# Kernel optimization log

Measured on AMD Instinct MI355X. Metric: run time of the kernel, lower is better.

## Reference

```python
import jax, jax.numpy as jnp
import numpy as np
import math

H = 128      # hidden_size
B = 4        # bsz
N = 32       # bsz * num_doc_per_q
L = 128      # doc_len


def setup_inputs() -> dict:
    key = jax.random.key(0)
    ks = jax.random.split(key, 7)
    word_ent_info = jax.random.normal(ks[0], (N, L, H), dtype=jnp.float32)
    word_ent_info_mask = jax.random.randint(ks[1], (N, L), 0, 2, dtype=jnp.int32)
    doc = jax.random.normal(ks[2], (N, L, H), dtype=jnp.float32)
    doc_mask = jax.random.randint(ks[3], (N, L), 0, 2, dtype=jnp.int32)
    q_for_text = jax.random.normal(ks[4], (B, H), dtype=jnp.float32)
    # nn.Linear(3H, H): weight [H, 3H], bias [H]
    W1 = jax.random.normal(ks[5], (H, 3 * H), dtype=jnp.float32) / math.sqrt(3 * H)
    b1 = jnp.zeros((H,), dtype=jnp.float32)
    # nn.Linear(H, 1): weight [1, H], bias [1]
    w2 = jax.random.normal(ks[6], (1, H), dtype=jnp.float32) / math.sqrt(H)
    b2 = jnp.zeros((1,), dtype=jnp.float32)
    return {"word_ent_info": word_ent_info, "word_ent_info_mask": word_ent_info_mask,
            "doc": doc, "doc_mask": doc_mask, "q_for_text": q_for_text,
            "W1": W1, "b1": b1, "w2": w2, "b2": b2}


def reference(word_ent_info, word_ent_info_mask, doc, doc_mask, q_for_text, W1, b1, w2, b2):
    n, l, h = doc.shape
    bsz = q_for_text.shape[0]
    dt = doc.dtype

    # word_ent_infoagg = mask^T @ word_ent_info -> [N, H]
    m = word_ent_info_mask.astype(dt)
    ent_agg = jnp.einsum('nl,nlh->nh', m, word_ent_info)

    # q expanded to one row per document: [N, H]
    q_exp = jnp.repeat(q_for_text, n // bsz, axis=0)

    # Split W1 over the concat([doc_self, ent_agg, q_agg]) feature axis.
    # score_pre[n,j,k,:] = W1a @ (doc_j*doc_k) + W1b @ (doc_j*ent_agg) + W1c @ (doc_k*q)
    W1a, W1b, W1c = jnp.split(W1, 3, axis=1)        # each [H, H]
    A = jnp.einsum('nje,nke,ge->njkg', doc, doc, W1a)          # [N,L,L,H]
    Bt = jnp.einsum('nje,ge->njg', doc * ent_agg[:, None, :], W1b)  # [N,L,H]
    Ct = jnp.einsum('nke,ge->nkg', doc * q_exp[:, None, :], W1c)    # [N,L,H]
    hid = jnp.tanh(A + Bt[:, :, None, :] + Ct[:, None, :, :] + b1)  # [N,L,L,H]

    score = (jnp.einsum('njkg,g->njk', hid, w2[0]) + b2[0]) / math.sqrt(h)

    dm = doc_mask.astype(dt)
    score_mask = dm[:, :, None] * dm[:, None, :]     # [N,L,L]
    score = jnp.where(score_mask == 0.0, jnp.asarray(-1e9, dt), score)
    w = jax.nn.softmax(score, axis=-1) * score_mask
    doc_ent_enc = jnp.einsum('njk,nkh->njh', w, doc)  # [N,L,H]
    return doc_ent_enc
```

## Files before the change

kernel.cpp:

```cpp
#include <hip/hip_runtime.h>
#include <hip/hip_bf16.h>
#include <math.h>

#define Hh 128
#define Nn 32
#define Ll 128
#define W1S 384
#define PAD 136

typedef __attribute__((ext_vector_type(8))) short short8;
typedef __attribute__((ext_vector_type(4))) float floatx4;

__device__ __forceinline__ unsigned short f2bf(float x) {
  __hip_bfloat16 h = __float2bfloat16(x);
  return __builtin_bit_cast(unsigned short, h);
}
__device__ __forceinline__ float bf2f(short s) {
  unsigned int u = ((unsigned int)(unsigned short)s) << 16;
  return __builtin_bit_cast(float, u);
}
__device__ __forceinline__ short8 pack8(float4 a, float4 b) {
  short8 r;
  r[0] = (short)f2bf(a.x); r[1] = (short)f2bf(a.y);
  r[2] = (short)f2bf(a.z); r[3] = (short)f2bf(a.w);
  r[4] = (short)f2bf(b.x); r[5] = (short)f2bf(b.y);
  r[6] = (short)f2bf(b.z); r[7] = (short)f2bf(b.w);
  return r;
}

__launch_bounds__(256, 1)
__global__ void k_prep(const float* __restrict__ wei, const int* __restrict__ wmask,
                       const float* __restrict__ doc, const float* __restrict__ q,
                       const float* __restrict__ W1,
                       float* __restrict__ Bt, float* __restrict__ Ct) {
  __shared__ __align__(16) short docb[Hh * PAD];
  __shared__ __align__(16) short Wb[Hh * PAD];
  __shared__ __align__(16) short Wc[Hh * PAD];
  __shared__ __align__(16) float entL[Hh];
  __shared__ __align__(16) float qL[Hh];
  __shared__ __align__(16) float red[2][Hh];

  int n = blockIdx.x, tid = threadIdx.x;
  const float* docn = doc + (size_t)n * Ll * Hh;
  int e8 = (tid & 15) * 8;

#pragma unroll
  for (int p = 0; p < 8; ++p) {
    int row = p * 16 + (tid >> 4);
    const float4* dp = (const float4*)(docn + (size_t)row * Hh + e8);
    *(short8*)(docb + row * PAD + e8) = pack8(dp[0], dp[1]);
    const float4* wbp = (const float4*)(W1 + (size_t)row * W1S + Hh + e8);
    *(short8*)(Wb + row * PAD + e8) = pack8(wbp[0], wbp[1]);
    const float4* wcp = (const float4*)(W1 + (size_t)row * W1S + 2 * Hh + e8);
    *(short8*)(Wc + row * PAD + e8) = pack8(wcp[0], wcp[1]);
  }
  {
    int e = tid & 127, half = tid >> 7;
    const float* wp = wei + (size_t)n * Ll * Hh + (size_t)half * 64 * Hh + e;
    const int* mp = wmask + n * Ll + half * 64;
    float a = 0.f;
#pragma unroll 8
    for (int l = 0; l < 64; ++l) a = fmaf((float)mp[l], wp[(size_t)l * Hh], a);
    red[half][e] = a;
  }
  if (tid < Hh) qL[tid] = q[(n >> 3) * Hh + tid];
  __syncthreads();
  if (tid < Hh) entL[tid] = red[0][tid] + red[1][tid];
  __syncthreads();

  int lane = tid & 63, w = tid >> 6;
  int l15 = lane & 15, quad = lane >> 4;

  float ef[32], qf[32];
#pragma unroll
  for (int c = 0; c < 4; ++c)
#pragma unroll
    for (int i = 0; i < 8; ++i) {
      int e = c * 32 + quad * 8 + i;
      ef[c * 8 + i] = entL[e];
      qf[c * 8 + i] = qL[e];
    }
  short8 draw[2][4];
#pragma unroll
  for (int mt = 0; mt < 2; ++mt)
#pragma unroll
    for (int c = 0; c < 4; ++c)
      draw[mt][c] = *(const short8*)(docb + (w * 32 + mt * 16 + l15) * PAD + c * 32 + quad * 8);

  for (int which = 0; which < 2; ++which) {
    const short* Ws = which ? Wc : Wb;
    const float* sf = which ? qf : ef;
    floatx4 acc[2][8];
#pragma unroll
    for (int mt = 0; mt < 2; ++mt)
#pragma unroll
      for (int nt = 0; nt < 8; ++nt) acc[mt][nt] = (floatx4){0.f, 0.f, 0.f, 0.f};
#pragma unroll
    for (int c = 0; c < 4; ++c) {
      short8 af[2];
#pragma unroll
      for (int mt = 0; mt < 2; ++mt) {
        float t[8];
#pragma unroll
        for (int i = 0; i < 8; ++i) t[i] = bf2f(draw[mt][c][i]) * sf[c * 8 + i];
        short8 r;
#pragma unroll
        for (int i = 0; i < 8; ++i) r[i] = (short)f2bf(t[i]);
        af[mt] = r;
      }
      short8 bfr[8];
#pragma unroll
      for (int nt = 0; nt < 8; ++nt)
        bfr[nt] = *(const short8*)(Ws + (nt * 16 + l15) * PAD + c * 32 + quad * 8);
#pragma unroll
      for (int mt = 0; mt < 2; ++mt)
#pragma unroll
        for (int nt = 0; nt < 8; ++nt)
          acc[mt][nt] = __builtin_amdgcn_mfma_f32_16x16x32_bf16(af[mt], bfr[nt], acc[mt][nt], 0, 0, 0);
    }
    float* outp = (which ? Ct : Bt) + (size_t)n * Ll * Hh;
#pragma unroll
    for (int mt = 0; mt < 2; ++mt)
#pragma unroll
      for (int nt = 0; nt < 8; ++nt)
#pragma unroll
        for (int r = 0; r < 4; ++r) {
          int k = w * 32 + mt * 16 + quad * 4 + r;
          outp[(size_t)k * Hh + nt * 16 + l15] = acc[mt][nt][r];
        }
  }
}

__launch_bounds__(256, 2)
__global__ void k_main(const float* __restrict__ doc, const int* __restrict__ dmask,
                       const float* __restrict__ W1, const float* __restrict__ b1,
                       const float* __restrict__ w2, const float* __restrict__ b2,
                       const float* __restrict__ Bt, const float* __restrict__ Ct,
                       float* __restrict__ out) {
  __shared__ __align__(16) short As[Hh * PAD];
  __shared__ __align__(16) short Bs[Hh * PAD];
  __shared__ __align__(16) float sc[Ll];
  __shared__ __align__(16) float scw[Ll];

  int bid = blockIdx.x;
  int n = bid & 31, j = bid >> 5;
  int tid = threadIdx.x;
  const float* docn = doc + (size_t)n * Ll * Hh;
  size_t orow = ((size_t)n * Ll + j) * Hh;

  if (dmask[n * Ll + j] == 0) {
    if (tid < Hh) out[orow + tid] = 0.f;
    return;
  }

  int e8 = (tid & 15) * 8;
  const float4* jp = (const float4*)(docn + (size_t)j * Hh + e8);
  float4 j0 = jp[0], j1 = jp[1];
#pragma unroll
  for (int p = 0; p < 8; ++p) {
    int row = p * 16 + (tid >> 4);
    const float4* wp = (const float4*)(W1 + (size_t)row * W1S + e8);
    *(short8*)(As + row * PAD + e8) = pack8(wp[0], wp[1]);
    const float4* dp = (const float4*)(docn + (size_t)row * Hh + e8);
    float4 d0 = dp[0], d1 = dp[1];
    d0.x *= j0.x; d0.y *= j0.y; d0.z *= j0.z; d0.w *= j0.w;
    d1.x *= j1.x; d1.y *= j1.y; d1.z *= j1.z; d1.w *= j1.w;
    *(short8*)(Bs + row * PAD + e8) = pack8(d0, d1);
  }
  __syncthreads();

  int lane = tid & 63, w = tid >> 6;
  int l15 = lane & 15, quad = lane >> 4;
  floatx4 acc[2][8];
#pragma unroll
  for (int mt = 0; mt < 2; ++mt)
#pragma unroll
    for (int nt = 0; nt < 8; ++nt) acc[mt][nt] = (floatx4){0.f, 0.f, 0.f, 0.f};
#pragma unroll
  for (int e0 = 0; e0 < Hh; e0 += 32) {
    int eo = e0 + quad * 8;
    short8 af[2], bfr[8];
    af[0] = *(const short8*)(Bs + (w * 32 + l15) * PAD + eo);
    af[1] = *(const short8*)(Bs + (w * 32 + 16 + l15) * PAD + eo);
#pragma unroll
    for (int nt = 0; nt < 8; ++nt)
      bfr[nt] = *(const short8*)(As + (nt * 16 + l15) * PAD + eo);
#pragma unroll
    for (int mt = 0; mt < 2; ++mt)
#pragma unroll
      for (int nt = 0; nt < 8; ++nt)
        acc[mt][nt] = __builtin_amdgcn_mfma_f32_16x16x32_bf16(af[mt], bfr[nt], acc[mt][nt], 0, 0, 0);
  }

  const float c2 = 2.885390081777927f;
  float bbc[8], w2r[8];
  const float* btrow = Bt + orow;
#pragma unroll
  for (int nt = 0; nt < 8; ++nt) {
    int g = nt * 16 + l15;
    bbc[nt] = (btrow[g] + b1[g]) * c2;
    w2r[nt] = w2[g];
  }
  const float* ctn = Ct + (size_t)n * Ll * Hh;
#pragma unroll
  for (int mt = 0; mt < 2; ++mt) {
#pragma unroll
    for (int r = 0; r < 4; ++r) {
      int k = w * 32 + mt * 16 + quad * 4 + r;
      const float* ctp = ctn + (size_t)k * Hh + l15;
      float p = 0.f;
#pragma unroll
      for (int nt = 0; nt < 8; ++nt) {
        float s = acc[mt][nt][r] + ctp[nt * 16];
        float a2 = fmaf(s, c2, bbc[nt]);
        float e = exp2f(a2);
        float th = fmaf(-2.f, __builtin_amdgcn_rcpf(e + 1.f), 1.f);
        p = fmaf(th, w2r[nt], p);
      }
      p += __shfl_xor(p, 1);
      p += __shfl_xor(p, 2);
      p += __shfl_xor(p, 4);
      p += __shfl_xor(p, 8);
      if (l15 == 0) sc[k] = p;
    }
  }
  __syncthreads();

  {
    float b2v = b2[0];
    const float inv = 0.088388347648318447f;
    const int* dmn = dmask + n * Ll;
    int m0 = dmn[lane], m1 = dmn[lane + 64];
    float s0 = (sc[lane] + b2v) * inv;
    float s1 = (sc[lane + 64] + b2v) * inv;
    s0 = m0 ? s0 : -1e9f;
    s1 = m1 ? s1 : -1e9f;
    float mx = fmaxf(s0, s1);
#pragma unroll
    for (int off = 32; off; off >>= 1) mx = fmaxf(mx, __shfl_xor(mx, off));
    float ex0 = __expf(s0 - mx), ex1 = __expf(s1 - mx);
    float sm = ex0 + ex1;
#pragma unroll
    for (int off = 32; off; off >>= 1) sm += __shfl_xor(sm, off);
    float rden = 1.f / sm;
    scw[lane] = m0 ? ex0 * rden : 0.f;
    scw[lane + 64] = m1 ? ex1 * rden : 0.f;
  }
  __syncthreads();

  float* ored = (float*)As;
  int half = tid >> 7, h = tid & 127;
  const float* dbase = docn + (size_t)half * 64 * Hh + h;
  float o = 0.f;
#pragma unroll 8
  for (int kk = 0; kk < 64; ++kk)
    o = fmaf(scw[half * 64 + kk], dbase[(size_t)kk * Hh], o);
  ored[half * Hh + h] = o;
  __syncthreads();
  if (tid < Ll) out[orow + tid] = ored[tid] + ored[Hh + tid];
}

extern "C" void kernel_launch(void* const* d_in, const int* in_sizes, int n_in,
                              void* d_out, int out_size, void* d_ws, size_t ws_size,
                              hipStream_t stream) {
  const float* wei   = (const float*)d_in[0];
  const int*   wmask = (const int*)d_in[1];
  const float* doc   = (const float*)d_in[2];
  const int*   dmask = (const int*)d_in[3];
  const float* q     = (const float*)d_in[4];
  const float* W1    = (const float*)d_in[5];
  const float* b1    = (const float*)d_in[6];
  const float* w2    = (const float*)d_in[7];
  const float* b2    = (const float*)d_in[8];
  float* out = (float*)d_out;

  float* ws = (float*)d_ws;
  float* Bt = ws;
  float* Ct = Bt + (size_t)Nn * Ll * Hh;

  k_prep<<<Nn, 256, 0, stream>>>(wei, wmask, doc, q, W1, Bt, Ct);
  k_main<<<Nn * Ll, 256, 0, stream>>>(doc, dmask, W1, b1, w2, b2, Bt, Ct, out);
}
```

Before: 136.3 us.

## Fold doc_j and q scaling into W1 operand, stream bf16 doc from global

The main kernel now scales W1a by doc_j (and W1c by q) in shared memory and multiplies against a bf16 copy of doc read straight from global memory. This folds the Ct term into the same MFMA accumulation and removes the per-block doc*doc_j staging and its shared buffer. The prep kernel is split four ways per document, writes the bf16 doc copy, and folds b1 into Bt. Shared memory per block drops, so occupancy is raised to 4 blocks. The cost is a second W1 staging pass per block and per-lane global loads of the doc fragments.

Result: slower. 219.4 us (+60.9%).

```diff
diff --git a/kernel.cpp b/kernel.cpp
--- a/kernel.cpp
+++ b/kernel.cpp
@@ -14,10 +14,6 @@
 __device__ __forceinline__ unsigned short f2bf(float x) {
   __hip_bfloat16 h = __float2bfloat16(x);
   return __builtin_bit_cast(unsigned short, h);
-}
-__device__ __forceinline__ float bf2f(short s) {
-  unsigned int u = ((unsigned int)(unsigned short)s) << 16;
-  return __builtin_bit_cast(float, u);
 }
 __device__ __forceinline__ short8 pack8(float4 a, float4 b) {
   short8 r;
@@ -27,32 +23,30 @@
   r[6] = (short)f2bf(b.z); r[7] = (short)f2bf(b.w);
   return r;
 }
-
-__launch_bounds__(256, 1)
+__device__ __forceinline__ void mul4(float4& a, const float4& b) {
+  a.x *= b.x; a.y *= b.y; a.z *= b.z; a.w *= b.w;
+}
+
+__launch_bounds__(256, 2)
 __global__ void k_prep(const float* __restrict__ wei, const int* __restrict__ wmask,
-                       const float* __restrict__ doc, const float* __restrict__ q,
-                       const float* __restrict__ W1,
-                       float* __restrict__ Bt, float* __restrict__ Ct) {
-  __shared__ __align__(16) short docb[Hh * PAD];
+                       const float* __restrict__ doc, const float* __restrict__ W1,
+                       const float* __restrict__ b1,
+                       float* __restrict__ Bt, short* __restrict__ docb) {
   __shared__ __align__(16) short Wb[Hh * PAD];
-  __shared__ __align__(16) short Wc[Hh * PAD];
-  __shared__ __align__(16) float entL[Hh];
-  __shared__ __align__(16) float qL[Hh];
+  __shared__ __align__(16) short Xs[32 * PAD];
   __shared__ __align__(16) float red[2][Hh];
 
-  int n = blockIdx.x, tid = threadIdx.x;
+  int bid = blockIdx.x;
+  int n = bid & 31, s = bid >> 5;
+  int tid = threadIdx.x;
   const float* docn = doc + (size_t)n * Ll * Hh;
-  int e8 = (tid & 15) * 8;
+  int e8 = (tid & 15) * 8, rsub = tid >> 4;
 
 #pragma unroll
   for (int p = 0; p < 8; ++p) {
-    int row = p * 16 + (tid >> 4);
-    const float4* dp = (const float4*)(docn + (size_t)row * Hh + e8);
-    *(short8*)(docb + row * PAD + e8) = pack8(dp[0], dp[1]);
-    const float4* wbp = (const float4*)(W1 + (size_t)row * W1S + Hh + e8);
-    *(short8*)(Wb + row * PAD + e8) = pack8(wbp[0], wbp[1]);
-    const float4* wcp = (const float4*)(W1 + (size_t)row * W1S + 2 * Hh + e8);
-    *(short8*)(Wc + row * PAD + e8) = pack8(wcp[0], wcp[1]);
+    int row = p * 16 + rsub;
+    const float4* wp = (const float4*)(W1 + (size_t)row * W1S + Hh + e8);
+    *(short8*)(Wb + row * PAD + e8) = pack8(wp[0], wp[1]);
   }
   {
     int e = tid & 127, half = tid >> 7;
@@ -63,83 +57,80 @@
     for (int l = 0; l < 64; ++l) a = fmaf((float)mp[l], wp[(size_t)l * Hh], a);
     red[half][e] = a;
   }
-  if (tid < Hh) qL[tid] = q[(n >> 3) * Hh + tid];
-  __syncthreads();
-  if (tid < Hh) entL[tid] = red[0][tid] + red[1][tid];
+  {
+    int row = s * 32 + (tid >> 3), c16 = (tid & 7) * 16;
+    const float4* dp = (const float4*)(docn + (size_t)row * Hh + c16);
+    float4 d0 = dp[0], d1 = dp[1], d2 = dp[2], d3 = dp[3];
+    short* ob = docb + ((size_t)n * Ll + row) * Hh + c16;
+    *(short8*)(ob) = pack8(d0, d1);
+    *(short8*)(ob + 8) = pack8(d2, d3);
+  }
+  __syncthreads();
+
+  float4 ent0, ent1;
+  {
+    float e0v[8];
+#pragma unroll
+    for (int i = 0; i < 8; ++i) e0v[i] = red[0][e8 + i] + red[1][e8 + i];
+    ent0 = make_float4(e0v[0], e0v[1], e0v[2], e0v[3]);
+    ent1 = make_float4(e0v[4], e0v[5], e0v[6], e0v[7]);
+  }
+#pragma unroll
+  for (int p = 0; p < 2; ++p) {
+    int row = p * 16 + rsub;
+    const float4* dp = (const float4*)(docn + (size_t)(s * 32 + row) * Hh + e8);
+    float4 a = dp[0], b = dp[1];
+    mul4(a, ent0); mul4(b, ent1);
+    *(short8*)(Xs + row * PAD + e8) = pack8(a, b);
+  }
   __syncthreads();
 
   int lane = tid & 63, w = tid >> 6;
   int l15 = lane & 15, quad = lane >> 4;
-
-  float ef[32], qf[32];
-#pragma unroll
-  for (int c = 0; c < 4; ++c)
-#pragma unroll
-    for (int i = 0; i < 8; ++i) {
-      int e = c * 32 + quad * 8 + i;
-      ef[c * 8 + i] = entL[e];
-      qf[c * 8 + i] = qL[e];
-    }
-  short8 draw[2][4];
+  floatx4 acc[2][2];
 #pragma unroll
   for (int mt = 0; mt < 2; ++mt)
 #pragma unroll
-    for (int c = 0; c < 4; ++c)
-      draw[mt][c] = *(const short8*)(docb + (w * 32 + mt * 16 + l15) * PAD + c * 32 + quad * 8);
-
-  for (int which = 0; which < 2; ++which) {
-    const short* Ws = which ? Wc : Wb;
-    const float* sf = which ? qf : ef;
-    floatx4 acc[2][8];
+    for (int nt = 0; nt < 2; ++nt) acc[mt][nt] = (floatx4){0.f, 0.f, 0.f, 0.f};
+#pragma unroll
+  for (int e0 = 0; e0 < Hh; e0 += 32) {
+    int eo = e0 + quad * 8;
+    short8 af[2], bfr[2];
 #pragma unroll
     for (int mt = 0; mt < 2; ++mt)
-#pragma unroll
-      for (int nt = 0; nt < 8; ++nt) acc[mt][nt] = (floatx4){0.f, 0.f, 0.f, 0.f};
-#pragma unroll
-    for (int c = 0; c < 4; ++c) {
-      short8 af[2];
-#pragma unroll
-      for (int mt = 0; mt < 2; ++mt) {
-        float t[8];
-#pragma unroll
-        for (int i = 0; i < 8; ++i) t[i] = bf2f(draw[mt][c][i]) * sf[c * 8 + i];
-        short8 r;
-#pragma unroll
-        for (int i = 0; i < 8; ++i) r[i] = (short)f2bf(t[i]);
-        af[mt] = r;
+      af[mt] = *(const short8*)(Xs + (mt * 16 + l15) * PAD + eo);
+#pragma unroll
+    for (int nt = 0; nt < 2; ++nt)
+      bfr[nt] = *(const short8*)(Wb + (w * 32 + nt * 16 + l15) * PAD + eo);
+#pragma unroll
+    for (int mt = 0; mt < 2; ++mt)
+#pragma unroll
+      for (int nt = 0; nt < 2; ++nt)
+        acc[mt][nt] = __builtin_amdgcn_mfma_f32_16x16x32_bf16(af[mt], bfr[nt], acc[mt][nt], 0, 0, 0);
+  }
+  float* btn = Bt + (size_t)n * Ll * Hh;
+  float b1g[2];
+#pragma unroll
+  for (int nt = 0; nt < 2; ++nt) b1g[nt] = b1[w * 32 + nt * 16 + l15];
+#pragma unroll
+  for (int mt = 0; mt < 2; ++mt)
+#pragma unroll
+    for (int nt = 0; nt < 2; ++nt)
+#pragma unroll
+      for (int r = 0; r < 4; ++r) {
+        int j = s * 32 + mt * 16 + quad * 4 + r;
+        btn[(size_t)j * Hh + w * 32 + nt * 16 + l15] = acc[mt][nt][r] + b1g[nt];
       }
-      short8 bfr[8];
-#pragma unroll
-      for (int nt = 0; nt < 8; ++nt)
-        bfr[nt] = *(const short8*)(Ws + (nt * 16 + l15) * PAD + c * 32 + quad * 8);
-#pragma unroll
-      for (int mt = 0; mt < 2; ++mt)
-#pragma unroll
-        for (int nt = 0; nt < 8; ++nt)
-          acc[mt][nt] = __builtin_amdgcn_mfma_f32_16x16x32_bf16(af[mt], bfr[nt], acc[mt][nt], 0, 0, 0);
-    }
-    float* outp = (which ? Ct : Bt) + (size_t)n * Ll * Hh;
-#pragma unroll
-    for (int mt = 0; mt < 2; ++mt)
-#pragma unroll
-      for (int nt = 0; nt < 8; ++nt)
-#pragma unroll
-        for (int r = 0; r < 4; ++r) {
-          int k = w * 32 + mt * 16 + quad * 4 + r;
-          outp[(size_t)k * Hh + nt * 16 + l15] = acc[mt][nt][r];
-        }
-  }
-}
-
-__launch_bounds__(256, 2)
+}
+
+__launch_bounds__(256, 4)
 __global__ void k_main(const float* __restrict__ doc, const int* __restrict__ dmask,
-                       const float* __restrict__ W1, const float* __restrict__ b1,
-                       const float* __restrict__ w2, const float* __restrict__ b2,
-                       const float* __restrict__ Bt, const float* __restrict__ Ct,
+                       const float* __restrict__ W1, const float* __restrict__ w2,
+                       const float* __restrict__ b2, const float* __restrict__ q,
+                       const float* __restrict__ Bt, const short* __restrict__ docb,
                        float* __restrict__ out) {
   __shared__ __align__(16) short As[Hh * PAD];
-  __shared__ __align__(16) short Bs[Hh * PAD];
-  __shared__ __align__(16) float sc[Ll];
+  __shared__ __align__(16) float scp[4][Ll];
   __shared__ __align__(16) float scw[Ll];
 
   int bid = blockIdx.x;
@@ -153,66 +144,92 @@
     return;
   }
 
-  int e8 = (tid & 15) * 8;
-  const float4* jp = (const float4*)(docn + (size_t)j * Hh + e8);
-  float4 j0 = jp[0], j1 = jp[1];
+  int e8 = (tid & 15) * 8, rsub = tid >> 4;
+  const float4* djp = (const float4*)(docn + (size_t)j * Hh + e8);
+  float4 dj0 = djp[0], dj1 = djp[1];
+
 #pragma unroll
   for (int p = 0; p < 8; ++p) {
-    int row = p * 16 + (tid >> 4);
+    int row = p * 16 + rsub;
     const float4* wp = (const float4*)(W1 + (size_t)row * W1S + e8);
-    *(short8*)(As + row * PAD + e8) = pack8(wp[0], wp[1]);
-    const float4* dp = (const float4*)(docn + (size_t)row * Hh + e8);
-    float4 d0 = dp[0], d1 = dp[1];
-    d0.x *= j0.x; d0.y *= j0.y; d0.z *= j0.z; d0.w *= j0.w;
-    d1.x *= j1.x; d1.y *= j1.y; d1.z *= j1.z; d1.w *= j1.w;
-    *(short8*)(Bs + row * PAD + e8) = pack8(d0, d1);
+    float4 a = wp[0], b = wp[1];
+    mul4(a, dj0); mul4(b, dj1);
+    *(short8*)(As + row * PAD + e8) = pack8(a, b);
   }
   __syncthreads();
 
   int lane = tid & 63, w = tid >> 6;
   int l15 = lane & 15, quad = lane >> 4;
-  floatx4 acc[2][8];
-#pragma unroll
-  for (int mt = 0; mt < 2; ++mt)
-#pragma unroll
-    for (int nt = 0; nt < 8; ++nt) acc[mt][nt] = (floatx4){0.f, 0.f, 0.f, 0.f};
+  const short* dbn = docb + (size_t)n * Ll * Hh;
+
+  floatx4 acc[8][2];
+#pragma unroll
+  for (int mt = 0; mt < 8; ++mt)
+#pragma unroll
+    for (int nt = 0; nt < 2; ++nt) acc[mt][nt] = (floatx4){0.f, 0.f, 0.f, 0.f};
+
 #pragma unroll
   for (int e0 = 0; e0 < Hh; e0 += 32) {
     int eo = e0 + quad * 8;
-    short8 af[2], bfr[8];
-    af[0] = *(const short8*)(Bs + (w * 32 + l15) * PAD + eo);
-    af[1] = *(const short8*)(Bs + (w * 32 + 16 + l15) * PAD + eo);
-#pragma unroll
-    for (int nt = 0; nt < 8; ++nt)
-      bfr[nt] = *(const short8*)(As + (nt * 16 + l15) * PAD + eo);
-#pragma unroll
-    for (int mt = 0; mt < 2; ++mt)
-#pragma unroll
-      for (int nt = 0; nt < 8; ++nt)
-        acc[mt][nt] = __builtin_amdgcn_mfma_f32_16x16x32_bf16(af[mt], bfr[nt], acc[mt][nt], 0, 0, 0);
+    short8 bfr[2];
+#pragma unroll
+    for (int nt = 0; nt < 2; ++nt)
+      bfr[nt] = *(const short8*)(As + (w * 32 + nt * 16 + l15) * PAD + eo);
+#pragma unroll
+    for (int mt = 0; mt < 8; ++mt) {
+      short8 af = *(const short8*)(dbn + (size_t)(mt * 16 + l15) * Hh + eo);
+#pragma unroll
+      for (int nt = 0; nt < 2; ++nt)
+        acc[mt][nt] = __builtin_amdgcn_mfma_f32_16x16x32_bf16(af, bfr[nt], acc[mt][nt], 0, 0, 0);
+    }
+  }
+  __syncthreads();
+
+  const float4* qp = (const float4*)(q + (size_t)(n >> 3) * Hh + e8);
+  float4 q0 = qp[0], q1 = qp[1];
+#pragma unroll
+  for (int p = 0; p < 8; ++p) {
+    int row = p * 16 + rsub;
+    const float4* wp = (const float4*)(W1 + (size_t)row * W1S + 2 * Hh + e8);
+    float4 a = wp[0], b = wp[1];
+    mul4(a, q0); mul4(b, q1);
+    *(short8*)(As + row * PAD + e8) = pack8(a, b);
+  }
+  __syncthreads();
+
+#pragma unroll
+  for (int e0 = 0; e0 < Hh; e0 += 32) {
+    int eo = e0 + quad * 8;
+    short8 bfr[2];
+#pragma unroll
+    for (int nt = 0; nt < 2; ++nt)
+      bfr[nt] = *(const short8*)(As + (w * 32 + nt * 16 + l15) * PAD + eo);
+#pragma unroll
+    for (int mt = 0; mt < 8; ++mt) {
+      short8 af = *(const short8*)(dbn + (size_t)(mt * 16 + l15) * Hh + eo);
+#pragma unroll
+      for (int nt = 0; nt < 2; ++nt)
+        acc[mt][nt] = __builtin_amdgcn_mfma_f32_16x16x32_bf16(af, bfr[nt], acc[mt][nt], 0, 0, 0);
+    }
   }
 
   const float c2 = 2.885390081777927f;
-  float bbc[8], w2r[8];
   const float* btrow = Bt + orow;
-#pragma unroll
-  for (int nt = 0; nt < 8; ++nt) {
-    int g = nt * 16 + l15;
-    bbc[nt] = (btrow[g] + b1[g]) * c2;
+  float bbc[2], w2r[2];
+#pragma unroll
+  for (int nt = 0; nt < 2; ++nt) {
+    int g = w * 32 + nt * 16 + l15;
+    bbc[nt] = btrow[g] * c2;
     w2r[nt] = w2[g];
   }
-  const float* ctn = Ct + (size_t)n * Ll * Hh;
-#pragma unroll
-  for (int mt = 0; mt < 2; ++mt) {
+#pragma unroll
+  for (int mt = 0; mt < 8; ++mt) {
 #pragma unroll
     for (int r = 0; r < 4; ++r) {
-      int k = w * 32 + mt * 16 + quad * 4 + r;
-      const float* ctp = ctn + (size_t)k * Hh + l15;
       float p = 0.f;
 #pragma unroll
-      for (int nt = 0; nt < 8; ++nt) {
-        float s = acc[mt][nt][r] + ctp[nt * 16];
-        float a2 = fmaf(s, c2, bbc[nt]);
+      for (int nt = 0; nt < 2; ++nt) {
+        float a2 = fmaf(acc[mt][nt][r], c2, bbc[nt]);
         float e = exp2f(a2);
         float th = fmaf(-2.f, __builtin_amdgcn_rcpf(e + 1.f), 1.f);
         p = fmaf(th, w2r[nt], p);
@@ -221,7 +238,7 @@
       p += __shfl_xor(p, 2);
       p += __shfl_xor(p, 4);
       p += __shfl_xor(p, 8);
-      if (l15 == 0) sc[k] = p;
+      if (l15 == 0) scp[w][mt * 16 + quad * 4 + r] = p;
     }
   }
   __syncthreads();
@@ -230,11 +247,12 @@
     float b2v = b2[0];
     const float inv = 0.088388347648318447f;
     const int* dmn = dmask + n * Ll;
-    int m0 = dmn[lane], m1 = dmn[lane + 64];
-    float s0 = (sc[lane] + b2v) * inv;
-    float s1 = (sc[lane + 64] + b2v) * inv;
-    s0 = m0 ? s0 : -1e9f;
-    s1 = m1 ? s1 : -1e9f;
+    int k0 = lane, k1 = lane + 64;
+    float s0 = scp[0][k0] + scp[1][k0] + scp[2][k0] + scp[3][k0];
+    float s1 = scp[0][k1] + scp[1][k1] + scp[2][k1] + scp[3][k1];
+    int m0 = dmn[k0], m1 = dmn[k1];
+    s0 = m0 ? (s0 + b2v) * inv : -1e9f;
+    s1 = m1 ? (s1 + b2v) * inv : -1e9f;
     float mx = fmaxf(s0, s1);
 #pragma unroll
     for (int off = 32; off; off >>= 1) mx = fmaxf(mx, __shfl_xor(mx, off));
@@ -243,12 +261,12 @@
 #pragma unroll
     for (int off = 32; off; off >>= 1) sm += __shfl_xor(sm, off);
     float rden = 1.f / sm;
-    scw[lane] = m0 ? ex0 * rden : 0.f;
-    scw[lane + 64] = m1 ? ex1 * rden : 0.f;
-  }
-  __syncthreads();
-
-  float* ored = (float*)As;
+    scw[k0] = m0 ? ex0 * rden : 0.f;
+    scw[k1] = m1 ? ex1 * rden : 0.f;
+  }
+  __syncthreads();
+
+  float* ored = (float*)scp;
   int half = tid >> 7, h = tid & 127;
   const float* dbase = docn + (size_t)half * 64 * Hh + h;
   float o = 0.f;
@@ -274,10 +292,10 @@
   const float* b2    = (const float*)d_in[8];
   float* out = (float*)d_out;
 
-  float* ws = (float*)d_ws;
-  float* Bt = ws;
-  float* Ct = Bt + (size_t)Nn * Ll * Hh;
-
-  k_prep<<<Nn, 256, 0, stream>>>(wei, wmask, doc, q, W1, Bt, Ct);
-  k_main<<<Nn * Ll, 256, 0, stream>>>(doc, dmask, W1, b1, w2, b2, Bt, Ct, out);
-}
+  float* ws   = (float*)d_ws;
+  float* Bt   = ws;
+  short* docb = (short*)(Bt + (size_t)Nn * Ll * Hh);
+
+  k_prep<<<4 * Nn, 256, 0, stream>>>(wei, wmask, doc, W1, b1, Bt, docb);
+  k_main<<<Nn * Ll, 256, 0, stream>>>(doc, dmask, W1, w2, b2, q, Bt, docb, out);
+}
```

## Process four query rows per block, pre-convert W1a to bf16, split prep kernel

Applied to the files above, without the earlier changes.

The main kernel now handles four j rows per block, loading the bf16 W1a tile once and reusing it across the four rows. The final weighted sum over doc reads each doc element once for all four rows. W1a is converted to bf16 once in the prep kernel and stored in workspace. The prep kernel is split into two blocks per document, one computing Bt (with b1 folded in) and one computing Ct, to double its parallelism. The cost is fewer main-kernel blocks (1024), less parallelism and more serialized work per block, including extra syncs per row.

After: 137.9 us. Within noise of the previous version (+1.2%).

```diff
diff --git a/kernel.cpp b/kernel.cpp
--- a/kernel.cpp
+++ b/kernel.cpp
@@ -14,10 +14,6 @@
 __device__ __forceinline__ unsigned short f2bf(float x) {
   __hip_bfloat16 h = __float2bfloat16(x);
   return __builtin_bit_cast(unsigned short, h);
-}
-__device__ __forceinline__ float bf2f(short s) {
-  unsigned int u = ((unsigned int)(unsigned short)s) << 16;
-  return __builtin_bit_cast(float, u);
 }
 __device__ __forceinline__ short8 pack8(float4 a, float4 b) {
   short8 r;
@@ -27,34 +23,28 @@
   r[6] = (short)f2bf(b.z); r[7] = (short)f2bf(b.w);
   return r;
 }
-
-__launch_bounds__(256, 1)
+__device__ __forceinline__ void mul4(float4& a, const float4& b) {
+  a.x *= b.x; a.y *= b.y; a.z *= b.z; a.w *= b.w;
+}
+
+__launch_bounds__(256, 2)
 __global__ void k_prep(const float* __restrict__ wei, const int* __restrict__ wmask,
                        const float* __restrict__ doc, const float* __restrict__ q,
-                       const float* __restrict__ W1,
-                       float* __restrict__ Bt, float* __restrict__ Ct) {
-  __shared__ __align__(16) short docb[Hh * PAD];
-  __shared__ __align__(16) short Wb[Hh * PAD];
-  __shared__ __align__(16) short Wc[Hh * PAD];
-  __shared__ __align__(16) float entL[Hh];
-  __shared__ __align__(16) float qL[Hh];
+                       const float* __restrict__ W1, const float* __restrict__ b1,
+                       float* __restrict__ Bt, float* __restrict__ Ct,
+                       short* __restrict__ W1ab) {
+  __shared__ __align__(16) short Xs[Hh * PAD];
+  __shared__ __align__(16) short Ws[Hh * PAD];
   __shared__ __align__(16) float red[2][Hh];
-
-  int n = blockIdx.x, tid = threadIdx.x;
+  __shared__ __align__(16) float ms[Hh];
+
+  int bid = blockIdx.x;
+  int n = bid >> 1, which = bid & 1;
+  int tid = threadIdx.x;
   const float* docn = doc + (size_t)n * Ll * Hh;
-  int e8 = (tid & 15) * 8;
-
-#pragma unroll
-  for (int p = 0; p < 8; ++p) {
-    int row = p * 16 + (tid >> 4);
-    const float4* dp = (const float4*)(docn + (size_t)row * Hh + e8);
-    *(short8*)(docb + row * PAD + e8) = pack8(dp[0], dp[1]);
-    const float4* wbp = (const float4*)(W1 + (size_t)row * W1S + Hh + e8);
-    *(short8*)(Wb + row * PAD + e8) = pack8(wbp[0], wbp[1]);
-    const float4* wcp = (const float4*)(W1 + (size_t)row * W1S + 2 * Hh + e8);
-    *(short8*)(Wc + row * PAD + e8) = pack8(wcp[0], wcp[1]);
-  }
-  {
+  int e8 = (tid & 15) * 8, rsub = tid >> 4;
+
+  if (which == 0) {
     int e = tid & 127, half = tid >> 7;
     const float* wp = wei + (size_t)n * Ll * Hh + (size_t)half * 64 * Hh + e;
     const int* mp = wmask + n * Ll + half * 64;
@@ -62,110 +52,37 @@
 #pragma unroll 8
     for (int l = 0; l < 64; ++l) a = fmaf((float)mp[l], wp[(size_t)l * Hh], a);
     red[half][e] = a;
-  }
-  if (tid < Hh) qL[tid] = q[(n >> 3) * Hh + tid];
-  __syncthreads();
-  if (tid < Hh) entL[tid] = red[0][tid] + red[1][tid];
-  __syncthreads();
-
-  int lane = tid & 63, w = tid >> 6;
-  int l15 = lane & 15, quad = lane >> 4;
-
-  float ef[32], qf[32];
-#pragma unroll
-  for (int c = 0; c < 4; ++c)
-#pragma unroll
-    for (int i = 0; i < 8; ++i) {
-      int e = c * 32 + quad * 8 + i;
-      ef[c * 8 + i] = entL[e];
-      qf[c * 8 + i] = qL[e];
-    }
-  short8 draw[2][4];
-#pragma unroll
-  for (int mt = 0; mt < 2; ++mt)
-#pragma unroll
-    for (int c = 0; c < 4; ++c)
-      draw[mt][c] = *(const short8*)(docb + (w * 32 + mt * 16 + l15) * PAD + c * 32 + quad * 8);
-
-  for (int which = 0; which < 2; ++which) {
-    const short* Ws = which ? Wc : Wb;
-    const float* sf = which ? qf : ef;
-    floatx4 acc[2][8];
-#pragma unroll
-    for (int mt = 0; mt < 2; ++mt)
-#pragma unroll
-      for (int nt = 0; nt < 8; ++nt) acc[mt][nt] = (floatx4){0.f, 0.f, 0.f, 0.f};
-#pragma unroll
-    for (int c = 0; c < 4; ++c) {
-      short8 af[2];
-#pragma unroll
-      for (int mt = 0; mt < 2; ++mt) {
-        float t[8];
-#pragma unroll
-        for (int i = 0; i < 8; ++i) t[i] = bf2f(draw[mt][c][i]) * sf[c * 8 + i];
-        short8 r;
-#pragma unroll
-        for (int i = 0; i < 8; ++i) r[i] = (short)f2bf(t[i]);
-        af[mt] = r;
-      }
-      short8 bfr[8];
-#pragma unroll
-      for (int nt = 0; nt < 8; ++nt)
-        bfr[nt] = *(const short8*)(Ws + (nt * 16 + l15) * PAD + c * 32 + quad * 8);
-#pragma unroll
-      for (int mt = 0; mt < 2; ++mt)
-#pragma unroll
-        for (int nt = 0; nt < 8; ++nt)
-          acc[mt][nt] = __builtin_amdgcn_mfma_f32_16x16x32_bf16(af[mt], bfr[nt], acc[mt][nt], 0, 0, 0);
-    }
-    float* outp = (which ? Ct : Bt) + (size_t)n * Ll * Hh;
-#pragma unroll
-    for (int mt = 0; mt < 2; ++mt)
-#pragma unroll
-      for (int nt = 0; nt < 8; ++nt)
-#pragma unroll
-        for (int r = 0; r < 4; ++r) {
-          int k = w * 32 + mt * 16 + quad * 4 + r;
-          outp[(size_t)k * Hh + nt * 16 + l15] = acc[mt][nt][r];
-        }
-  }
-}
-
-__launch_bounds__(256, 2)
-__global__ void k_main(const float* __restrict__ doc, const int* __restrict__ dmask,
-                       const float* __restrict__ W1, const float* __restrict__ b1,
-                       const float* __restrict__ w2, const float* __restrict__ b2,
-                       const float* __restrict__ Bt, const float* __restrict__ Ct,
-                       float* __restrict__ out) {
-  __shared__ __align__(16) short As[Hh * PAD];
-  __shared__ __align__(16) short Bs[Hh * PAD];
-  __shared__ __align__(16) float sc[Ll];
-  __shared__ __align__(16) float scw[Ll];
-
-  int bid = blockIdx.x;
-  int n = bid & 31, j = bid >> 5;
-  int tid = threadIdx.x;
-  const float* docn = doc + (size_t)n * Ll * Hh;
-  size_t orow = ((size_t)n * Ll + j) * Hh;
-
-  if (dmask[n * Ll + j] == 0) {
-    if (tid < Hh) out[orow + tid] = 0.f;
-    return;
-  }
-
-  int e8 = (tid & 15) * 8;
-  const float4* jp = (const float4*)(docn + (size_t)j * Hh + e8);
-  float4 j0 = jp[0], j1 = jp[1];
+  } else {
+    if (tid < Hh) ms[tid] = q[(size_t)(n >> 3) * Hh + tid];
+  }
+  if (tid < 32) {
+    int row = which * 64 + n * 2 + (tid >> 4);
+    int c8 = (tid & 15) * 8;
+    const float4* wp = (const float4*)(W1 + (size_t)row * W1S + c8);
+    *(short8*)(W1ab + row * Hh + c8) = pack8(wp[0], wp[1]);
+  }
+  const float* wbase = W1 + Hh + which * Hh;
 #pragma unroll
   for (int p = 0; p < 8; ++p) {
-    int row = p * 16 + (tid >> 4);
-    const float4* wp = (const float4*)(W1 + (size_t)row * W1S + e8);
-    *(short8*)(As + row * PAD + e8) = pack8(wp[0], wp[1]);
-    const float4* dp = (const float4*)(docn + (size_t)row * Hh + e8);
-    float4 d0 = dp[0], d1 = dp[1];
-    d0.x *= j0.x; d0.y *= j0.y; d0.z *= j0.z; d0.w *= j0.w;
-    d1.x *= j1.x; d1.y *= j1.y; d1.z *= j1.z; d1.w *= j1.w;
-    *(short8*)(Bs + row * PAD + e8) = pack8(d0, d1);
+    int row = p * 16 + rsub;
+    const float4* wp = (const float4*)(wbase + (size_t)row * W1S + e8);
+    *(short8*)(Ws + row * PAD + e8) = pack8(wp[0], wp[1]);
+  }
+  __syncthreads();
+  if (which == 0 && tid < Hh) ms[tid] = red[0][tid] + red[1][tid];
+  __syncthreads();
+
+  {
+    const float4* mp4 = (const float4*)(ms + e8);
+    float4 m0 = mp4[0], m1 = mp4[1];
+#pragma unroll
+    for (int p = 0; p < 8; ++p) {
+      int row = p * 16 + rsub;
+      const float4* dp = (const float4*)(docn + (size_t)row * Hh + e8);
+      float4 a = dp[0], b = dp[1];
+      mul4(a, m0); mul4(b, m1);
+      *(short8*)(Xs + row * PAD + e8) = pack8(a, b);
+    }
   }
   __syncthreads();
 
@@ -180,84 +97,172 @@
   for (int e0 = 0; e0 < Hh; e0 += 32) {
     int eo = e0 + quad * 8;
     short8 af[2], bfr[8];
-    af[0] = *(const short8*)(Bs + (w * 32 + l15) * PAD + eo);
-    af[1] = *(const short8*)(Bs + (w * 32 + 16 + l15) * PAD + eo);
+    af[0] = *(const short8*)(Xs + (w * 32 + l15) * PAD + eo);
+    af[1] = *(const short8*)(Xs + (w * 32 + 16 + l15) * PAD + eo);
 #pragma unroll
     for (int nt = 0; nt < 8; ++nt)
-      bfr[nt] = *(const short8*)(As + (nt * 16 + l15) * PAD + eo);
+      bfr[nt] = *(const short8*)(Ws + (nt * 16 + l15) * PAD + eo);
 #pragma unroll
     for (int mt = 0; mt < 2; ++mt)
 #pragma unroll
       for (int nt = 0; nt < 8; ++nt)
         acc[mt][nt] = __builtin_amdgcn_mfma_f32_16x16x32_bf16(af[mt], bfr[nt], acc[mt][nt], 0, 0, 0);
   }
-
+  float* outp = (which ? Ct : Bt) + (size_t)n * Ll * Hh;
+  float addv[8];
+#pragma unroll
+  for (int nt = 0; nt < 8; ++nt) addv[nt] = which ? 0.f : b1[nt * 16 + l15];
+#pragma unroll
+  for (int mt = 0; mt < 2; ++mt)
+#pragma unroll
+    for (int nt = 0; nt < 8; ++nt)
+#pragma unroll
+      for (int r = 0; r < 4; ++r) {
+        int k = w * 32 + mt * 16 + quad * 4 + r;
+        outp[(size_t)k * Hh + nt * 16 + l15] = acc[mt][nt][r] + addv[nt];
+      }
+}
+
+__launch_bounds__(256, 2)
+__global__ void k_main(const float* __restrict__ doc, const int* __restrict__ dmask,
+                       const short* __restrict__ W1ab, const float* __restrict__ w2,
+                       const float* __restrict__ b2,
+                       const float* __restrict__ Bt, const float* __restrict__ Ct,
+                       float* __restrict__ out) {
+  __shared__ __align__(16) short Bg[Hh * PAD];
+  __shared__ __align__(16) short Adj[Hh * PAD];
+  __shared__ __align__(16) float sc[Ll];
+  __shared__ __align__(16) float scwq[Ll][4];
+  __shared__ __align__(16) float ored[2][4][Hh];
+
+  int bid = blockIdx.x;
+  int n = bid & 31, jq = bid >> 5;
+  int tid = threadIdx.x;
+  const float* docn = doc + (size_t)n * Ll * Hh;
+  const int* dmn = dmask + n * Ll;
+  int e8 = (tid & 15) * 8, rsub = tid >> 4;
+
+#pragma unroll
+  for (int p = 0; p < 8; ++p) {
+    int row = p * 16 + rsub;
+    *(short8*)(Bg + row * PAD + e8) = *(const short8*)(W1ab + row * Hh + e8);
+  }
+
+  int lane = tid & 63, w = tid >> 6;
+  int l15 = lane & 15, quad = lane >> 4;
   const float c2 = 2.885390081777927f;
-  float bbc[8], w2r[8];
-  const float* btrow = Bt + orow;
-#pragma unroll
-  for (int nt = 0; nt < 8; ++nt) {
-    int g = nt * 16 + l15;
-    bbc[nt] = (btrow[g] + b1[g]) * c2;
-    w2r[nt] = w2[g];
-  }
+  const float inv = 0.088388347648318447f;
+  float b2v = b2[0];
+  float w2r[8];
+#pragma unroll
+  for (int nt = 0; nt < 8; ++nt) w2r[nt] = w2[nt * 16 + l15];
   const float* ctn = Ct + (size_t)n * Ll * Hh;
-#pragma unroll
-  for (int mt = 0; mt < 2; ++mt) {
-#pragma unroll
-    for (int r = 0; r < 4; ++r) {
-      int k = w * 32 + mt * 16 + quad * 4 + r;
-      const float* ctp = ctn + (size_t)k * Hh + l15;
-      float p = 0.f;
-#pragma unroll
-      for (int nt = 0; nt < 8; ++nt) {
-        float s = acc[mt][nt][r] + ctp[nt * 16];
-        float a2 = fmaf(s, c2, bbc[nt]);
-        float e = exp2f(a2);
-        float th = fmaf(-2.f, __builtin_amdgcn_rcpf(e + 1.f), 1.f);
-        p = fmaf(th, w2r[nt], p);
+  int m0 = dmn[lane], m1 = dmn[lane + 64];
+
+  for (int jv = 0; jv < 4; ++jv) {
+    int j = jq * 4 + jv;
+    if (dmn[j] == 0) {
+      if (tid < Ll) scwq[tid][jv] = 0.f;
+      continue;
+    }
+    {
+      const float4* djp = (const float4*)(docn + (size_t)j * Hh + e8);
+      float4 dj0 = djp[0], dj1 = djp[1];
+#pragma unroll
+      for (int p = 0; p < 8; ++p) {
+        int row = p * 16 + rsub;
+        const float4* dp = (const float4*)(docn + (size_t)row * Hh + e8);
+        float4 a = dp[0], b = dp[1];
+        mul4(a, dj0); mul4(b, dj1);
+        *(short8*)(Adj + row * PAD + e8) = pack8(a, b);
       }
-      p += __shfl_xor(p, 1);
-      p += __shfl_xor(p, 2);
-      p += __shfl_xor(p, 4);
-      p += __shfl_xor(p, 8);
-      if (l15 == 0) sc[k] = p;
-    }
-  }
-  __syncthreads();
-
-  {
-    float b2v = b2[0];
-    const float inv = 0.088388347648318447f;
-    const int* dmn = dmask + n * Ll;
-    int m0 = dmn[lane], m1 = dmn[lane + 64];
-    float s0 = (sc[lane] + b2v) * inv;
-    float s1 = (sc[lane + 64] + b2v) * inv;
-    s0 = m0 ? s0 : -1e9f;
-    s1 = m1 ? s1 : -1e9f;
-    float mx = fmaxf(s0, s1);
-#pragma unroll
-    for (int off = 32; off; off >>= 1) mx = fmaxf(mx, __shfl_xor(mx, off));
-    float ex0 = __expf(s0 - mx), ex1 = __expf(s1 - mx);
-    float sm = ex0 + ex1;
-#pragma unroll
-    for (int off = 32; off; off >>= 1) sm += __shfl_xor(sm, off);
-    float rden = 1.f / sm;
-    scw[lane] = m0 ? ex0 * rden : 0.f;
-    scw[lane + 64] = m1 ? ex1 * rden : 0.f;
-  }
-  __syncthreads();
-
-  float* ored = (float*)As;
+    }
+    __syncthreads();
+
+    floatx4 acc[2][8];
+#pragma unroll
+    for (int mt = 0; mt < 2; ++mt)
+#pragma unroll
+      for (int nt = 0; nt < 8; ++nt) acc[mt][nt] = (floatx4){0.f, 0.f, 0.f, 0.f};
+#pragma unroll
+    for (int e0 = 0; e0 < Hh; e0 += 32) {
+      int eo = e0 + quad * 8;
+      short8 af[2], bfr[8];
+      af[0] = *(const short8*)(Adj + (w * 32 + l15) * PAD + eo);
+      af[1] = *(const short8*)(Adj + (w * 32 + 16 + l15) * PAD + eo);
+#pragma unroll
+      for (int nt = 0; nt < 8; ++nt)
+        bfr[nt] = *(const short8*)(Bg + (nt * 16 + l15) * PAD + eo);
+#pragma unroll
+      for (int mt = 0; mt < 2; ++mt)
+#pragma unroll
+        for (int nt = 0; nt < 8; ++nt)
+          acc[mt][nt] = __builtin_amdgcn_mfma_f32_16x16x32_bf16(af[mt], bfr[nt], acc[mt][nt], 0, 0, 0);
+    }
+
+    const float* btrow = Bt + ((size_t)n * Ll + j) * Hh;
+    float bbc[8];
+#pragma unroll
+    for (int nt = 0; nt < 8; ++nt) bbc[nt] = btrow[nt * 16 + l15] * c2;
+#pragma unroll
+    for (int mt = 0; mt < 2; ++mt) {
+#pragma unroll
+      for (int r = 0; r < 4; ++r) {
+        int k = w * 32 + mt * 16 + quad * 4 + r;
+        const float* ctp = ctn + (size_t)k * Hh + l15;
+        float p = 0.f;
+#pragma unroll
+        for (int nt = 0; nt < 8; ++nt) {
+          float s = acc[mt][nt][r] + ctp[nt * 16];
+          float a2 = fmaf(s, c2, bbc[nt]);
+          float e = exp2f(a2);
+          float th = fmaf(-2.f, __builtin_amdgcn_rcpf(e + 1.f), 1.f);
+          p = fmaf(th, w2r[nt], p);
+        }
+        p += __shfl_xor(p, 1);
+        p += __shfl_xor(p, 2);
+        p += __shfl_xor(p, 4);
+        p += __shfl_xor(p, 8);
+        if (l15 == 0) sc[k] = p;
+      }
+    }
+    __syncthreads();
+
+    {
+      float s0 = m0 ? (sc[lane] + b2v) * inv : -1e9f;
+      float s1 = m1 ? (sc[lane + 64] + b2v) * inv : -1e9f;
+      float mx = fmaxf(s0, s1);
+#pragma unroll
+      for (int off = 32; off; off >>= 1) mx = fmaxf(mx, __shfl_xor(mx, off));
+      float ex0 = __expf(s0 - mx), ex1 = __expf(s1 - mx);
+      float sm = ex0 + ex1;
+#pragma unroll
+      for (int off = 32; off; off >>= 1) sm += __shfl_xor(sm, off);
+      float rden = 1.f / sm;
+      scwq[lane][jv] = m0 ? ex0 * rden : 0.f;
+      scwq[lane + 64][jv] = m1 ? ex1 * rden : 0.f;
+    }
+  }
+  __syncthreads();
+
   int half = tid >> 7, h = tid & 127;
   const float* dbase = docn + (size_t)half * 64 * Hh + h;
-  float o = 0.f;
+  float o0 = 0.f, o1 = 0.f, o2 = 0.f, o3 = 0.f;
 #pragma unroll 8
-  for (int kk = 0; kk < 64; ++kk)
-    o = fmaf(scw[half * 64 + kk], dbase[(size_t)kk * Hh], o);
-  ored[half * Hh + h] = o;
-  __syncthreads();
-  if (tid < Ll) out[orow + tid] = ored[tid] + ored[Hh + tid];
+  for (int kk = 0; kk < 64; ++kk) {
+    float d = dbase[(size_t)kk * Hh];
+    float4 wv = *(const float4*)&scwq[half * 64 + kk][0];
+    o0 = fmaf(wv.x, d, o0); o1 = fmaf(wv.y, d, o1);
+    o2 = fmaf(wv.z, d, o2); o3 = fmaf(wv.w, d, o3);
+  }
+  ored[half][0][h] = o0; ored[half][1][h] = o1;
+  ored[half][2][h] = o2; ored[half][3][h] = o3;
+  __syncthreads();
+  if (tid < Ll) {
+#pragma unroll
+    for (int jv = 0; jv < 4; ++jv)
+      out[((size_t)n * Ll + jq * 4 + jv) * Hh + tid] = ored[0][jv][tid] + ored[1][jv][tid];
+  }
 }
 
 extern "C" void kernel_launch(void* const* d_in, const int* in_sizes, int n_in,
@@ -274,10 +279,11 @@
   const float* b2    = (const float*)d_in[8];
   float* out = (float*)d_out;
 
-  float* ws = (float*)d_ws;
-  float* Bt = ws;
-  float* Ct = Bt + (size_t)Nn * Ll * Hh;
-
-  k_prep<<<Nn, 256, 0, stream>>>(wei, wmask, doc, q, W1, Bt, Ct);
-  k_main<<<Nn * Ll, 256, 0, stream>>>(doc, dmask, W1, b1, w2, b2, Bt, Ct, out);
-}
+  float* ws   = (float*)d_ws;
+  float* Bt   = ws;
+  float* Ct   = Bt + (size_t)Nn * Ll * Hh;
+  short* W1ab = (short*)(Ct + (size_t)Nn * Ll * Hh);
+
+  k_prep<<<2 * Nn, 256, 0, stream>>>(wei, wmask, doc, q, W1, b1, Bt, Ct, W1ab);
+  k_main<<<Nn * Ll / 4, 256, 0, stream>>>(doc, dmask, W1ab, w2, b2, Bt, Ct, out);
+}
```
